# Optimization experiments

Measured on AMD Instinct MI355X. Metric: run time of the kernel, lower is better.

The kernel has to match this reference:

```python
import jax, jax.numpy as jnp
import numpy as np

B, C, H, W = 16, 32, 32, 2048


def setup_inputs() -> dict:
    key = jax.random.key(0)
    ks = jax.random.split(key, 7)
    s = 1.0 / np.sqrt(C * H)  # torch conv2d default init scale (fan_in = C*H*1)
    x = jax.random.normal(ks[0], (B, C, H, W), dtype=jnp.float32)
    wq = jax.random.uniform(ks[1], (C, C, H), jnp.float32, -s, s)
    bq = jax.random.uniform(ks[2], (C,), jnp.float32, -s, s)
    wk = jax.random.uniform(ks[3], (C, C, H), jnp.float32, -s, s)
    bk = jax.random.uniform(ks[4], (C,), jnp.float32, -s, s)
    wv = jax.random.uniform(ks[5], (C, C, H), jnp.float32, -s, s)
    bv = jax.random.uniform(ks[6], (C,), jnp.float32, -s, s)
    return {"x": x, "wq": wq, "bq": bq, "wk": wk, "bk": bk, "wv": wv, "bv": bv}


def _proj(x, w, b):
    # Conv2d kernel (H,1) with no padding == contract over (in_channels, H).
    # x: [B,C,H,W], w: [Cout,Cin,H] -> [B,Cout,W]
    return jnp.einsum('bihw,oih->bow', x, w) + b[None, :, None]


def reference(x, wq, bq, wk, bk, wv, bv):
    q = _proj(x, wq, bq)            # [B,C,W]
    k = _proj(x, wk, bk)            # [B,C,W]
    v = _proj(x, wv, bv)            # [B,C,W]
    # query.permute(0,2,1) @ key -> [B,W,W]; NOTE: unscaled, as in source.
    scores = jnp.einsum('bcw,bcv->bwv', q, k)
    attn = jax.nn.softmax(scores, axis=-1)
    # value @ attention^T -> [B,C,W]
    out = jnp.einsum('bcv,bwv->bcw', v, attn)
    # bilinear upsample (1,W)->(H,W), align_corners=False: width is identity,
    # height replicates the single row -> pure broadcast. Then residual add.
    return out[:, :, None, :] + x
```

## Files before the change

### kernel.cpp

```cpp
#include <hip/hip_runtime.h>
#include <hip/hip_bf16.h>

typedef __bf16 bf16x8 __attribute__((ext_vector_type(8)));
typedef float  f32x4  __attribute__((ext_vector_type(4)));
typedef float  f32x16 __attribute__((ext_vector_type(16)));

#define NB 16
#define NC 32
#define NH 32
#define NW 2048
#define NK (NC*NH)

static __device__ __forceinline__ unsigned int pk2(float a, float b) {
    union { __bf16 h[2]; unsigned int u; } z;
    z.h[0] = (__bf16)a; z.h[1] = (__bf16)b;
    return z.u;
}

__global__ __launch_bounds__(256) void wprep_kernel(
    const float* __restrict__ wq, const float* __restrict__ wk,
    const float* __restrict__ wv, __bf16* __restrict__ wb)
{
    const int i = blockIdx.x * 256 + threadIdx.x;
    const float* srcs[3] = { wq, wk, wv };
    const float4 v = *(const float4*)(srcs[i >> 13] + (size_t)(i & 8191) * 4);
    union { __bf16 h[4]; unsigned long long u; } z;
    z.h[0] = (__bf16)v.x; z.h[1] = (__bf16)v.y;
    z.h[2] = (__bf16)v.z; z.h[3] = (__bf16)v.w;
    *(unsigned long long*)(wb + (size_t)i * 4) = z.u;
}

__global__ __launch_bounds__(256) void proj_kernel(
    const float* __restrict__ x, const __bf16* __restrict__ wb,
    const float* __restrict__ bq, const float* __restrict__ bk,
    const float* __restrict__ bv,
    __bf16* __restrict__ qT, __bf16* __restrict__ kT, __bf16* __restrict__ V)
{
    const int b    = blockIdx.x >> 6;
    const int wt   = blockIdx.x & 63;
    const int wave = threadIdx.x >> 6;
    const int lane = threadIdx.x & 63;
    const int g    = lane >> 4;
    const int lr   = lane & 15;
    const int w0   = wt * 32;

    const float* xb = x + (size_t)b * NK * NW;
    const int k0 = wave * 256;
    const float* xcol = xb + (w0 + 2*lr);

    f32x4 acc[2][6];
    #pragma unroll
    for (int mt = 0; mt < 2; ++mt)
        #pragma unroll
        for (int nt = 0; nt < 6; ++nt)
            acc[mt][nt] = f32x4{0.f, 0.f, 0.f, 0.f};

    float2 A0[8], A1[8];

#define LOADA(DST, KK)                                                        \
    _Pragma("unroll")                                                         \
    for (int j = 0; j < 8; ++j)                                               \
        DST[j] = *(const float2*)(xcol + (size_t)((KK) + g*8 + j) * NW);

#define COMPUTE(SRC, KK)                                                      \
    {                                                                         \
        bf16x8 af0, af1;                                                      \
        _Pragma("unroll")                                                     \
        for (int j = 0; j < 8; ++j) { af0[j] = (__bf16)SRC[j].x;              \
                                      af1[j] = (__bf16)SRC[j].y; }            \
        bf16x8 bfv[6];                                                        \
        _Pragma("unroll")                                                     \
        for (int nt = 0; nt < 6; ++nt)                                        \
            bfv[nt] = *(const bf16x8*)(wb + (size_t)(nt >> 1) * 32768         \
                                          + (size_t)((nt & 1) * 16 + lr) * NK \
                                          + (KK) + g*8);                      \
        _Pragma("unroll")                                                     \
        for (int nt = 0; nt < 6; ++nt) {                                      \
            acc[0][nt] = __builtin_amdgcn_mfma_f32_16x16x32_bf16(             \
                af0, bfv[nt], acc[0][nt], 0, 0, 0);                           \
            acc[1][nt] = __builtin_amdgcn_mfma_f32_16x16x32_bf16(             \
                af1, bfv[nt], acc[1][nt], 0, 0, 0);                           \
        }                                                                     \
    }

    LOADA(A0, k0);
    #pragma unroll
    for (int kp = 0; kp < 4; ++kp) {
        const int kk0 = k0 + (2*kp)     * 32;
        const int kk1 = k0 + (2*kp + 1) * 32;
        LOADA(A1, kk1);
        COMPUTE(A0, kk0);
        if (kp < 3) { LOADA(A0, kk1 + 32); }
        COMPUTE(A1, kk1);
    }
#undef LOADA
#undef COMPUTE

    __shared__ f32x4 part[4][6][64];
    const float* biases[3] = { bq, bk, bv };
    #pragma unroll
    for (int mt = 0; mt < 2; ++mt) {
        if (mt) __syncthreads();
        #pragma unroll
        for (int nt = 0; nt < 6; ++nt)
            part[wave][nt][lane] = acc[mt][nt];
        __syncthreads();
        #pragma unroll
        for (int q = 0; q < 2; ++q) {
            const int nt = wave + q * 4;
            if (nt < 6) {
                f32x4 s = part[0][nt][lane];
                #pragma unroll
                for (int sl = 1; sl < 4; ++sl) s += part[sl][nt][lane];
                const int pid = nt >> 1;
                const int o   = (nt & 1) * 16 + lr;
                const float bb = biases[pid][o];
                if (pid < 2) {
                    __bf16* dst = (pid ? kT : qT) + (size_t)b * NW * NC;
                    #pragma unroll
                    for (int r = 0; r < 4; ++r) {
                        const int w = w0 + 2*(g*4 + r) + mt;
                        dst[(size_t)w * NC + o] = (__bf16)(s[r] + bb);
                    }
                } else {
                    __bf16* dst = V + ((size_t)b * NC + o) * NW;
                    #pragma unroll
                    for (int r = 0; r < 4; ++r) {
                        const int w = w0 + 2*(g*4 + r) + mt;
                        dst[w] = (__bf16)(s[r] + bb);
                    }
                }
            }
        }
    }
}

__global__ __launch_bounds__(512) void attn_kernel(
    const float* __restrict__ x,
    const __bf16* __restrict__ qT, const __bf16* __restrict__ kT,
    const __bf16* __restrict__ V,
    float* __restrict__ out)
{
    const int b    = blockIdx.x >> 6;
    const int wt   = blockIdx.x & 63;
    const int w0   = wt * 32;
    const int wave = threadIdx.x >> 6;
    const int lane = threadIdx.x & 63;
    const int wl = lane & 31, hi = lane >> 5;
    const int swl = (wl & 0x13) | ((wl & 4) << 1) | ((wl & 8) >> 1);

    const __bf16* qTb = qT + (size_t)b * NW * NC;
    const __bf16* kTb = kT + (size_t)b * NW * NC;
    const __bf16* Vb  = V  + (size_t)b * NC * NW;

    const __bf16* qrow = qTb + (size_t)(w0 + wl) * NC;
    const bf16x8 qf0 = *(const bf16x8*)(qrow + hi*8);
    const bf16x8 qf1 = *(const bf16x8*)(qrow + 16 + hi*8);

    f32x16 acc, z16;
    #pragma unroll
    for (int r = 0; r < 16; ++r) { acc[r] = 0.f; z16[r] = 0.f; }
    float m = -1e30f, lsum = 0.f;

    const int vbeg = wave * 256;
    for (int it = 0; it < 8; ++it) {
        const int v0 = vbeg + it * 32;
        const __bf16* krow = kTb + (size_t)(v0 + swl) * NC;
        const bf16x8 kf0 = *(const bf16x8*)(krow + hi*8);
        const bf16x8 kf1 = *(const bf16x8*)(krow + 16 + hi*8);
        const __bf16* vrow = Vb + (size_t)wl * NW + v0;
        const bf16x8 vf0 = *(const bf16x8*)(vrow + hi*8);
        const bf16x8 vf1 = *(const bf16x8*)(vrow + 16 + hi*8);

        f32x16 s = __builtin_amdgcn_mfma_f32_32x32x16_bf16(kf0, qf0, z16, 0, 0, 0);
        s = __builtin_amdgcn_mfma_f32_32x32x16_bf16(kf1, qf1, s, 0, 0, 0);

        float tm[8];
        #pragma unroll
        for (int r = 0; r < 8; ++r) tm[r] = fmaxf(s[r], s[r+8]);
        #pragma unroll
        for (int r = 0; r < 4; ++r) tm[r] = fmaxf(tm[r], tm[r+4]);
        float vm = fmaxf(fmaxf(tm[0], tm[1]), fmaxf(tm[2], tm[3]));
        vm = fmaxf(vm, __shfl_xor(vm, 32));
        const float nm = fmaxf(m, vm);
        const float sc = __expf(m - nm);
        float p[16];
        #pragma unroll
        for (int r = 0; r < 16; ++r) p[r] = __expf(s[r] - nm);
        float ts[8];
        #pragma unroll
        for (int r = 0; r < 8; ++r) ts[r] = p[r] + p[r+8];
        #pragma unroll
        for (int r = 0; r < 4; ++r) ts[r] += ts[r+4];
        float ps = (ts[0] + ts[1]) + (ts[2] + ts[3]);
        ps += __shfl_xor(ps, 32);
        lsum = lsum * sc + ps;
        m = nm;
        #pragma unroll
        for (int r = 0; r < 16; ++r) acc[r] *= sc;

        union { unsigned int u[4]; bf16x8 v; } pf1, pf2;
        #pragma unroll
        for (int i = 0; i < 4; ++i) pf1.u[i] = pk2(p[2*i],     p[2*i + 1]);
        #pragma unroll
        for (int i = 0; i < 4; ++i) pf2.u[i] = pk2(p[8 + 2*i], p[8 + 2*i + 1]);

        acc = __builtin_amdgcn_mfma_f32_32x32x16_bf16(vf0, pf1.v, acc, 0, 0, 0);
        acc = __builtin_amdgcn_mfma_f32_32x32x16_bf16(vf1, pf2.v, acc, 0, 0, 0);
    }

    __shared__ float sm[8][32];
    __shared__ float sl[8][32];
    __shared__ float sO[8][32][33];
    __shared__ float Of[32][33];

    if (hi == 0) { sm[wave][wl] = m; sl[wave][wl] = lsum; }
    #pragma unroll
    for (int r = 0; r < 16; ++r) {
        const int c = (r & 3) + 8*(r >> 2) + 4*hi;
        sO[wave][c][wl] = acc[r];
    }
    __syncthreads();

    {
        const int w  = threadIdx.x & 31;
        const int c0 = (threadIdx.x >> 5) * 2;
        float ms[8], ls[8], f[8];
        #pragma unroll
        for (int s = 0; s < 8; ++s) { ms[s] = sm[s][w]; ls[s] = sl[s][w]; }
        float M = ms[0];
        #pragma unroll
        for (int s = 1; s < 8; ++s) M = fmaxf(M, ms[s]);
        float L = 0.f;
        #pragma unroll
        for (int s = 0; s < 8; ++s) { f[s] = __expf(ms[s] - M); L += ls[s] * f[s]; }
        const float rL = 1.0f / L;
        #pragma unroll
        for (int cc = 0; cc < 2; ++cc) {
            float o = 0.f;
            #pragma unroll
            for (int s = 0; s < 8; ++s) o += sO[s][c0 + cc][w] * f[s];
            Of[c0 + cc][w] = o * rL;
        }
    }
    __syncthreads();

    const float* xb = x   + (size_t)b * NC * NH * NW + w0;
    float*       ob = out + (size_t)b * NC * NH * NW + w0;
    const int chunk = threadIdx.x & 7;
    #pragma unroll
    for (int it = 0; it < 16; ++it) {
        const int row = it*64 + (threadIdx.x >> 3);
        const int c = row >> 5, h = row & 31;
        const size_t off = ((size_t)c * NH + h) * NW + chunk*4;
        const float4 xv = *(const float4*)(xb + off);
        float4 ov;
        ov.x = Of[c][chunk*4 + 0] + xv.x;
        ov.y = Of[c][chunk*4 + 1] + xv.y;
        ov.z = Of[c][chunk*4 + 2] + xv.z;
        ov.w = Of[c][chunk*4 + 3] + xv.w;
        *(float4*)(ob + off) = ov;
    }
}

extern "C" void kernel_launch(void* const* d_in, const int* in_sizes, int n_in,
                              void* d_out, int out_size, void* d_ws, size_t ws_size,
                              hipStream_t stream)
{
    const float* x  = (const float*)d_in[0];
    const float* wq = (const float*)d_in[1];
    const float* bq = (const float*)d_in[2];
    const float* wk = (const float*)d_in[3];
    const float* bk = (const float*)d_in[4];
    const float* wv = (const float*)d_in[5];
    const float* bv = (const float*)d_in[6];
    float* out = (float*)d_out;

    char* ws = (char*)d_ws;
    __bf16* qT = (__bf16*)(ws);
    __bf16* kT = (__bf16*)(ws + (2u << 20));
    __bf16* V  = (__bf16*)(ws + (4u << 20));
    __bf16* wb = (__bf16*)(ws + (6u << 20));

    hipLaunchKernelGGL(wprep_kernel, dim3(96), dim3(256), 0, stream, wq, wk, wv, wb);
    hipLaunchKernelGGL(proj_kernel, dim3(NB * 64), dim3(256), 0, stream,
                       x, wb, bq, bk, bv, qT, kT, V);
    hipLaunchKernelGGL(attn_kernel, dim3(NB * 64), dim3(512), 0, stream,
                       x, qT, kT, V, out);
}
```

Before: 102.9 us.

## Stage x tiles through LDS with coalesced float4 loads in projection kernel

Projection kernel now loads x with coalesced float4 reads (8 lanes across 32 columns), converts to bf16 and transposes through a per-wave double-buffered LDS stage, then reads MFMA A fragments as bf16x8 from LDS. This replaces strided float2 loads per lane, which were poorly coalesced. The w mapping changes to contiguous columns, so V stores become single 8-byte writes. The cost is extra LDS traffic and shared memory reused between the stage and the partial-sum buffer, which needs an added sync.

```diff
diff --git a/kernel.cpp b/kernel.cpp
--- a/kernel.cpp
+++ b/kernel.cpp
@@ -44,9 +44,16 @@
     const int lr   = lane & 15;
     const int w0   = wt * 32;
 
+    __shared__ __align__(16) char smem_raw[24576];
+    __bf16 (*stage)[2][32][40] = reinterpret_cast<__bf16(*)[2][32][40]>(smem_raw);
+    f32x4 (*part)[6][64] = reinterpret_cast<f32x4(*)[6][64]>(smem_raw);
+
     const float* xb = x + (size_t)b * NK * NW;
     const int k0 = wave * 256;
-    const float* xcol = xb + (w0 + 2*lr);
+
+    const int skr = lane >> 3;
+    const int swq = lane & 7;
+    const float* xs = xb + w0 + swq * 4;
 
     f32x4 acc[2][6];
     #pragma unroll
@@ -55,19 +62,28 @@
         for (int nt = 0; nt < 6; ++nt)
             acc[mt][nt] = f32x4{0.f, 0.f, 0.f, 0.f};
 
-    float2 A0[8], A1[8];
-
-#define LOADA(DST, KK)                                                        \
+    float4 xv[4];
+
+#define LOADX(STEP)                                                           \
     _Pragma("unroll")                                                         \
-    for (int j = 0; j < 8; ++j)                                               \
-        DST[j] = *(const float2*)(xcol + (size_t)((KK) + g*8 + j) * NW);
-
-#define COMPUTE(SRC, KK)                                                      \
+    for (int r4 = 0; r4 < 4; ++r4)                                            \
+        xv[r4] = *(const float4*)(xs + (size_t)(k0 + (STEP)*32 + r4*8 + skr) * NW);
+
+#define WRITEX(BUF)                                                           \
+    _Pragma("unroll")                                                         \
+    for (int r4 = 0; r4 < 4; ++r4) {                                          \
+        const int kl = r4*8 + skr;                                            \
+        __bf16* wp = &stage[wave][BUF][swq*4][kl];                            \
+        wp[0]   = (__bf16)xv[r4].x;                                           \
+        wp[40]  = (__bf16)xv[r4].y;                                           \
+        wp[80]  = (__bf16)xv[r4].z;                                           \
+        wp[120] = (__bf16)xv[r4].w;                                           \
+    }
+
+#define COMPUTE(BUF, KK)                                                      \
     {                                                                         \
-        bf16x8 af0, af1;                                                      \
-        _Pragma("unroll")                                                     \
-        for (int j = 0; j < 8; ++j) { af0[j] = (__bf16)SRC[j].x;              \
-                                      af1[j] = (__bf16)SRC[j].y; }            \
+        const bf16x8 af0 = *(const bf16x8*)&stage[wave][BUF][lr][g*8];        \
+        const bf16x8 af1 = *(const bf16x8*)&stage[wave][BUF][16 + lr][g*8];   \
         bf16x8 bfv[6];                                                        \
         _Pragma("unroll")                                                     \
         for (int nt = 0; nt < 6; ++nt)                                        \
@@ -83,24 +99,23 @@
         }                                                                     \
     }
 
-    LOADA(A0, k0);
-    #pragma unroll
-    for (int kp = 0; kp < 4; ++kp) {
-        const int kk0 = k0 + (2*kp)     * 32;
-        const int kk1 = k0 + (2*kp + 1) * 32;
-        LOADA(A1, kk1);
-        COMPUTE(A0, kk0);
-        if (kp < 3) { LOADA(A0, kk1 + 32); }
-        COMPUTE(A1, kk1);
-    }
-#undef LOADA
+    LOADX(0); WRITEX(0);
+    LOADX(1);
+    #pragma unroll
+    for (int s = 0; s < 8; ++s) {
+        const int cb = s & 1;
+        if (s < 7) { WRITEX(cb ^ 1); }
+        if (s < 6) { LOADX(s + 2); }
+        COMPUTE(cb, k0 + s*32);
+    }
+#undef LOADX
+#undef WRITEX
 #undef COMPUTE
 
-    __shared__ f32x4 part[4][6][64];
     const float* biases[3] = { bq, bk, bv };
     #pragma unroll
     for (int mt = 0; mt < 2; ++mt) {
-        if (mt) __syncthreads();
+        __syncthreads();
         #pragma unroll
         for (int nt = 0; nt < 6; ++nt)
             part[wave][nt][lane] = acc[mt][nt];
@@ -119,16 +134,15 @@
                     __bf16* dst = (pid ? kT : qT) + (size_t)b * NW * NC;
                     #pragma unroll
                     for (int r = 0; r < 4; ++r) {
-                        const int w = w0 + 2*(g*4 + r) + mt;
+                        const int w = w0 + mt*16 + g*4 + r;
                         dst[(size_t)w * NC + o] = (__bf16)(s[r] + bb);
                     }
                 } else {
-                    __bf16* dst = V + ((size_t)b * NC + o) * NW;
+                    union { __bf16 h[4]; unsigned long long u; } z;
                     #pragma unroll
-                    for (int r = 0; r < 4; ++r) {
-                        const int w = w0 + 2*(g*4 + r) + mt;
-                        dst[w] = (__bf16)(s[r] + bb);
-                    }
+                    for (int r = 0; r < 4; ++r) z.h[r] = (__bf16)(s[r] + bb);
+                    __bf16* dst = V + ((size_t)b * NC + o) * NW + (w0 + mt*16 + g*4);
+                    *(unsigned long long*)dst = z.u;
                 }
             }
         }
```

Measured after the change: 101.9 us. No clear change (-0.9%).
